# Kernel optimization log

Hardware: AMD Instinct MI355X
Metric: run time of the kernel (lower is better)

The kernel has to match this reference:

```python
import jax, jax.numpy as jnp
import numpy as np
import math

B, L, K = 2, 2048, 32
N_BINS = 37          # linspace(2.0, 20.0, 37)
N_ATOMS = 5          # N, CA, C, O, virtual CB
D_PE = 64            # relative position encoding dim
EDGE_DIM = 64        # config.edge_features_dim
EDGE_IN = N_ATOMS * N_ATOMS * N_BINS + D_PE  # 989 (source's 249 is a bug)


def _normalize(v):
    # matches F.normalize(dim=-1): v / max(||v||, eps)
    n = jnp.linalg.norm(v, axis=-1, keepdims=True)
    return v / jnp.maximum(n, 1e-12)


def setup_inputs() -> dict:
    key = jax.random.key(0)
    k1, k2, k3 = jax.random.split(key, 3)
    coordinates = jax.random.normal(k1, (B, L, 4, 3), dtype=jnp.float32)
    neighbor_indices = jax.random.randint(k2, (B, L, K), 0, L)
    W_edge = jax.random.normal(k3, (EDGE_IN, EDGE_DIM), dtype=jnp.float32) * 0.02
    b_edge = jnp.zeros((EDGE_DIM,), dtype=jnp.float32)
    return {"coordinates": coordinates, "neighbor_indices": neighbor_indices,
            "W_edge": W_edge, "b_edge": b_edge}


def reference(coordinates, neighbor_indices, W_edge, b_edge):
    dtype = coordinates.dtype
    Bsz, Lsz, Ksz = neighbor_indices.shape

    # ---- virtual CB (GeometricFeatures.compute_virtual_cb) ----
    n_c, ca, c_c = coordinates[:, :, 0], coordinates[:, :, 1], coordinates[:, :, 2]
    ca_n = _normalize(n_c - ca)
    ca_c = _normalize(c_c - ca)
    bisector = _normalize(ca_n + ca_c)
    perpendicular = _normalize(jnp.cross(ca_n, ca_c))
    cb_dir = _normalize(-bisector + 0.5 * perpendicular)
    virtual_cb = ca + 1.54 * cb_dir
    all_coords = jnp.concatenate([coordinates, virtual_cb[:, :, None]], axis=2)  # [B,L,5,3]

    # ---- sparse k-NN atom-pair distances (no O(L^2) intermediates) ----
    # gather neighbor atom coords: [B,L,K,5,3]
    nb_coords = jax.vmap(lambda x, i: x[i])(all_coords, neighbor_indices)
    # d[b,l,k,i,j] = || all_coords[b,l,i] - nb_coords[b,l,k,j] ||, pair order (i,j) matches the source loop
    diff = all_coords[:, :, None, :, None, :] - nb_coords[:, :, :, None, :, :]
    dists = jnp.linalg.norm(diff, axis=-1)  # [B,L,K,5,5]

    # ---- bucketize (torch.bucketize, right=False == searchsorted side='left') + clamp + one-hot ----
    bins = jnp.linspace(2.0, 20.0, N_BINS).astype(dtype)
    idx = jnp.clip(jnp.searchsorted(bins, dists, side='left'), 0, N_BINS - 1)
    onehot = jax.nn.one_hot(idx, N_BINS, dtype=dtype)  # [B,L,K,5,5,37]
    dist_feat = onehot.reshape(Bsz, Lsz, Ksz, N_ATOMS * N_ATOMS * N_BINS)  # [B,L,K,925]

    # ---- sinusoidal relative position encoding (d_model=64, clamp +-32) ----
    rel = neighbor_indices - jnp.arange(Lsz)[None, :, None]
    rel = jnp.clip(rel, -32, 32).astype(dtype)[..., None]  # [B,L,K,1]
    div_term = jnp.exp(jnp.arange(0, D_PE, 2).astype(dtype) * (-math.log(10000.0) / D_PE))
    ang = rel * div_term  # [B,L,K,32]
    pe = jnp.stack([jnp.sin(ang), jnp.cos(ang)], axis=-1).reshape(Bsz, Lsz, Ksz, D_PE)

    # ---- edge projection: split W to avoid materializing the 989-dim concat ----
    W_dist = W_edge[:N_ATOMS * N_ATOMS * N_BINS]  # [925, 64]
    W_pe = W_edge[N_ATOMS * N_ATOMS * N_BINS:]    # [64, 64]
    out = jnp.einsum('blkf,fh->blkh', dist_feat, W_dist) \
        + jnp.einsum('blkp,ph->blkh', pe, W_pe) + b_edge
    return out  # [B,L,K,EDGE_DIM]
```

## Files before the change

kernel.cpp:

```cpp
#include <hip/hip_runtime.h>
#include <math.h>

#pragma clang fp contract(off)

#define B_      2
#define L_      2048
#define K_      32
#define NBINS   37
#define H_      64
#define WD_ROWS 925
#define ITEMS   32

__device__ __forceinline__ float sqrt_f32_exact(float s) {
  return (float)sqrt((double)s);
}

__device__ __forceinline__ void norm3f(float& x, float& y, float& z) {
  float s = (x*x + y*y) + z*z;
  float n = sqrt_f32_exact(s);
  n = fmaxf(n, 1e-12f);
  x = x / n; y = y / n; z = z / n;
}

__global__ void pew_kernel(const float* __restrict__ W_edge,
                           const float* __restrict__ b_edge,
                           float* __restrict__ peW) {
  __shared__ double pe[64];
  const int r = blockIdx.x;
  const int h = threadIdx.x;
  if (h < 32) {
    const double c = -log(10000.0) / 64.0;
    const double ang = (double)(r - 32) * exp((double)(2 * h) * c);
    pe[2*h]     = sin(ang);
    pe[2*h + 1] = cos(ang);
  }
  __syncthreads();
  double acc = (double)b_edge[h];
  for (int j = 0; j < 64; ++j)
    acc += pe[j] * (double)W_edge[(WD_ROWS + j) * H_ + h];
  peW[r * H_ + h] = (float)acc;
}

__global__ __launch_bounds__(256) void edge_kernel(
    const float* __restrict__ coords,
    const int*   __restrict__ nbr,
    const float* __restrict__ W_edge,
    const float* __restrict__ peW,
    float*       __restrict__ out)
{
  __shared__ float          atoms[2 * ITEMS][5][3];
  __shared__ unsigned short fidx[ITEMS][25];
  __shared__ int            relid[ITEMS];

  const int t  = threadIdx.x;
  const int g0 = blockIdx.x * ITEMS;

  if (t < 2 * ITEMS) {
    const int i  = t >> 1;
    const int g  = g0 + i;
    const int b  = g / (L_ * K_);
    const int lk = g - b * (L_ * K_);
    const int l  = lk / K_;
    const int nb = nbr[g];
    const int res = (t & 1) ? nb : l;
    const float* cp = coords + (size_t)(b * L_ + res) * 12;
    float a[4][3];
    #pragma unroll
    for (int q = 0; q < 4; ++q)
      #pragma unroll
      for (int d = 0; d < 3; ++d)
        a[q][d] = cp[q * 3 + d];

    float nx = a[0][0]-a[1][0], ny = a[0][1]-a[1][1], nz = a[0][2]-a[1][2];
    float cx = a[2][0]-a[1][0], cy = a[2][1]-a[1][1], cz = a[2][2]-a[1][2];
    norm3f(nx, ny, nz);
    norm3f(cx, cy, cz);
    float bx = nx + cx, by = ny + cy, bz = nz + cz;
    norm3f(bx, by, bz);
    float px = ny*cz - nz*cy, py = nz*cx - nx*cz, pz = nx*cy - ny*cx;
    norm3f(px, py, pz);
    float dx = -bx + 0.5f*px, dy = -by + 0.5f*py, dz = -bz + 0.5f*pz;
    norm3f(dx, dy, dz);

    #pragma unroll
    for (int q = 0; q < 4; ++q)
      #pragma unroll
      for (int d = 0; d < 3; ++d)
        atoms[t][q][d] = a[q][d];
    atoms[t][4][0] = a[1][0] + 1.54f * dx;
    atoms[t][4][1] = a[1][1] + 1.54f * dy;
    atoms[t][4][2] = a[1][2] + 1.54f * dz;

    if ((t & 1) == 0) {
      int rel = nb - l;
      rel = rel < -32 ? -32 : (rel > 32 ? 32 : rel);
      relid[i] = rel + 32;
    }
  }
  __syncthreads();

  for (int task = t; task < ITEMS * 25; task += 256) {
    const int i  = task / 25;
    const int p  = task - i * 25;
    const int a1 = p / 5, a2 = p - a1 * 5;
    const float dx = atoms[2*i][a1][0] - atoms[2*i + 1][a2][0];
    const float dy = atoms[2*i][a1][1] - atoms[2*i + 1][a2][1];
    const float dz = atoms[2*i][a1][2] - atoms[2*i + 1][a2][2];
    const float d2 = (dx*dx + dy*dy) + dz*dz;
    const float d  = sqrt_f32_exact(d2);
    int m = (int)ceilf((d - 2.0f) * 2.0f);
    if (m < 0)  m = 0;
    if (m > NBINS) m = NBINS;
    while (m < NBINS && (2.0f + 0.5f * (float)m) < d) ++m;
    while (m > 0 && !((2.0f + 0.5f * (float)(m - 1)) < d)) --m;
    const int idx = m < (NBINS - 1) ? m : (NBINS - 1);
    fidx[i][p] = (unsigned short)(p * NBINS + idx);
  }
  __syncthreads();

  {
    const int i  = t >> 3;
    const int hq = (t & 7) * 8;
    const int g  = g0 + i;

    const float4* pw = (const float4*)(peW + relid[i] * H_ + hq);
    const float4 p0 = pw[0], p1 = pw[1];
    float acc[8] = {p0.x, p0.y, p0.z, p0.w, p1.x, p1.y, p1.z, p1.w};

    #pragma unroll 5
    for (int p = 0; p < 25; ++p) {
      const int f = fidx[i][p];
      const float4* wr = (const float4*)(W_edge + (size_t)f * H_ + hq);
      const float4 w0 = wr[0], w1 = wr[1];
      acc[0] += w0.x; acc[1] += w0.y; acc[2] += w0.z; acc[3] += w0.w;
      acc[4] += w1.x; acc[5] += w1.y; acc[6] += w1.z; acc[7] += w1.w;
    }

    float4* po = (float4*)(out + (size_t)g * H_ + hq);
    po[0] = make_float4(acc[0], acc[1], acc[2], acc[3]);
    po[1] = make_float4(acc[4], acc[5], acc[6], acc[7]);
  }
}

extern "C" void kernel_launch(void* const* d_in, const int* in_sizes, int n_in,
                              void* d_out, int out_size, void* d_ws, size_t ws_size,
                              hipStream_t stream) {
  const float* coords = (const float*)d_in[0];
  const int*   nbr    = (const int*)d_in[1];
  const float* W      = (const float*)d_in[2];
  const float* bvec   = (const float*)d_in[3];
  float*       out    = (float*)d_out;
  float*       peW    = (float*)d_ws;

  pew_kernel<<<65, 64, 0, stream>>>(W, bvec, peW);
  edge_kernel<<<(B_ * L_ * K_) / ITEMS, 256, 0, stream>>>(coords, nbr, W, peW, out);
}
```

Baseline: 101.7 us.

## Precompute per-residue virtual-CB atom table once and gather it in edge kernel

Virtual CB computation (with several double-precision sqrts) moves out of the per-edge kernel into a prep kernel that runs once per residue and writes a padded 16-float atom row to workspace. The peW table build is folded into the same launch. The edge kernel now processes one residue per block: it loads the center row once and gathers 32 neighbor rows as float4s. This removes the redundant per-edge CB recomputation at the cost of an extra workspace round trip and a block mapping tied to K=32.

```diff
diff --git a/kernel.cpp b/kernel.cpp
--- a/kernel.cpp
+++ b/kernel.cpp
@@ -9,7 +9,7 @@
 #define NBINS   37
 #define H_      64
 #define WD_ROWS 925
-#define ITEMS   32
+#define NRES    (B_ * L_)
 
 __device__ __forceinline__ float sqrt_f32_exact(float s) {
   return (float)sqrt((double)s);
@@ -22,48 +22,36 @@
   x = x / n; y = y / n; z = z / n;
 }
 
-__global__ void pew_kernel(const float* __restrict__ W_edge,
-                           const float* __restrict__ b_edge,
-                           float* __restrict__ peW) {
-  __shared__ double pe[64];
-  const int r = blockIdx.x;
-  const int h = threadIdx.x;
-  if (h < 32) {
-    const double c = -log(10000.0) / 64.0;
-    const double ang = (double)(r - 32) * exp((double)(2 * h) * c);
-    pe[2*h]     = sin(ang);
-    pe[2*h + 1] = cos(ang);
-  }
-  __syncthreads();
-  double acc = (double)b_edge[h];
-  for (int j = 0; j < 64; ++j)
-    acc += pe[j] * (double)W_edge[(WD_ROWS + j) * H_ + h];
-  peW[r * H_ + h] = (float)acc;
-}
-
-__global__ __launch_bounds__(256) void edge_kernel(
+__global__ __launch_bounds__(256) void prep_kernel(
     const float* __restrict__ coords,
-    const int*   __restrict__ nbr,
     const float* __restrict__ W_edge,
-    const float* __restrict__ peW,
-    float*       __restrict__ out)
+    const float* __restrict__ b_edge,
+    float*       __restrict__ peW,
+    float*       __restrict__ allc)
 {
-  __shared__ float          atoms[2 * ITEMS][5][3];
-  __shared__ unsigned short fidx[ITEMS][25];
-  __shared__ int            relid[ITEMS];
-
-  const int t  = threadIdx.x;
-  const int g0 = blockIdx.x * ITEMS;
-
-  if (t < 2 * ITEMS) {
-    const int i  = t >> 1;
-    const int g  = g0 + i;
-    const int b  = g / (L_ * K_);
-    const int lk = g - b * (L_ * K_);
-    const int l  = lk / K_;
-    const int nb = nbr[g];
-    const int res = (t & 1) ? nb : l;
-    const float* cp = coords + (size_t)(b * L_ + res) * 12;
+  const int t = threadIdx.x;
+  if (blockIdx.x < 17) {
+    __shared__ double pe[4][64];
+    const int row = t >> 6;
+    const int r   = blockIdx.x * 4 + row;
+    const int h   = t & 63;
+    if (r < 65 && h < 32) {
+      const double c = -log(10000.0) / 64.0;
+      const double ang = (double)(r - 32) * exp((double)(2 * h) * c);
+      pe[row][2*h]     = sin(ang);
+      pe[row][2*h + 1] = cos(ang);
+    }
+    __syncthreads();
+    if (r < 65) {
+      double acc = (double)b_edge[h];
+      for (int j = 0; j < 64; ++j)
+        acc += pe[row][j] * (double)W_edge[(WD_ROWS + j) * H_ + h];
+      peW[r * H_ + h] = (float)acc;
+    }
+  } else {
+    const int res = (blockIdx.x - 17) * 256 + t;
+    if (res >= NRES) return;
+    const float* cp = coords + (size_t)res * 12;
     float a[4][3];
     #pragma unroll
     for (int q = 0; q < 4; ++q)
@@ -82,16 +70,51 @@
     float dx = -bx + 0.5f*px, dy = -by + 0.5f*py, dz = -bz + 0.5f*pz;
     norm3f(dx, dy, dz);
 
+    float row[16];
     #pragma unroll
     for (int q = 0; q < 4; ++q)
       #pragma unroll
       for (int d = 0; d < 3; ++d)
-        atoms[t][q][d] = a[q][d];
-    atoms[t][4][0] = a[1][0] + 1.54f * dx;
-    atoms[t][4][1] = a[1][1] + 1.54f * dy;
-    atoms[t][4][2] = a[1][2] + 1.54f * dz;
+        row[q * 3 + d] = a[q][d];
+    row[12] = a[1][0] + 1.54f * dx;
+    row[13] = a[1][1] + 1.54f * dy;
+    row[14] = a[1][2] + 1.54f * dz;
+    row[15] = 0.0f;
 
-    if ((t & 1) == 0) {
+    float4* o = (float4*)(allc + (size_t)res * 16);
+    o[0] = make_float4(row[0],  row[1],  row[2],  row[3]);
+    o[1] = make_float4(row[4],  row[5],  row[6],  row[7]);
+    o[2] = make_float4(row[8],  row[9],  row[10], row[11]);
+    o[3] = make_float4(row[12], row[13], row[14], row[15]);
+  }
+}
+
+__global__ __launch_bounds__(256) void edge_kernel(
+    const int*   __restrict__ nbr,
+    const float* __restrict__ allc,
+    const float* __restrict__ W_edge,
+    const float* __restrict__ peW,
+    float*       __restrict__ out)
+{
+  __shared__ float          center[16];
+  __shared__ float          natoms[K_][16];
+  __shared__ unsigned short fidx[K_][25];
+  __shared__ int            relid[K_];
+
+  const int t   = threadIdx.x;
+  const int bl  = blockIdx.x;
+  const int l   = bl & (L_ - 1);
+  const int g0  = bl * K_;
+
+  if (t < 4) {
+    ((float4*)center)[t] = ((const float4*)(allc + (size_t)bl * 16))[t];
+  }
+  if (t < 4 * K_) {
+    const int i = t >> 2, c = t & 3;
+    const int nb = nbr[g0 + i];
+    const int brow = (bl & ~(L_ - 1)) + nb;
+    ((float4*)natoms[i])[c] = ((const float4*)(allc + (size_t)brow * 16))[c];
+    if (c == 0) {
       int rel = nb - l;
       rel = rel < -32 ? -32 : (rel > 32 ? 32 : rel);
       relid[i] = rel + 32;
@@ -99,13 +122,13 @@
   }
   __syncthreads();
 
-  for (int task = t; task < ITEMS * 25; task += 256) {
+  for (int task = t; task < K_ * 25; task += 256) {
     const int i  = task / 25;
     const int p  = task - i * 25;
     const int a1 = p / 5, a2 = p - a1 * 5;
-    const float dx = atoms[2*i][a1][0] - atoms[2*i + 1][a2][0];
-    const float dy = atoms[2*i][a1][1] - atoms[2*i + 1][a2][1];
-    const float dz = atoms[2*i][a1][2] - atoms[2*i + 1][a2][2];
+    const float dx = center[a1 * 3 + 0] - natoms[i][a2 * 3 + 0];
+    const float dy = center[a1 * 3 + 1] - natoms[i][a2 * 3 + 1];
+    const float dz = center[a1 * 3 + 2] - natoms[i][a2 * 3 + 2];
     const float d2 = (dx*dx + dy*dy) + dz*dz;
     const float d  = sqrt_f32_exact(d2);
     int m = (int)ceilf((d - 2.0f) * 2.0f);
@@ -151,7 +174,8 @@
   const float* bvec   = (const float*)d_in[3];
   float*       out    = (float*)d_out;
   float*       peW    = (float*)d_ws;
+  float*       allc   = (float*)((char*)d_ws + 32768);
 
-  pew_kernel<<<65, 64, 0, stream>>>(W, bvec, peW);
-  edge_kernel<<<(B_ * L_ * K_) / ITEMS, 256, 0, stream>>>(coords, nbr, W, peW, out);
+  prep_kernel<<<33, 256, 0, stream>>>(coords, W, bvec, peW, allc);
+  edge_kernel<<<NRES, 256, 0, stream>>>(nbr, allc, W, peW, out);
 }
```

Result: no change. 100.9 us (-0.8%).
